# Optimization experiments

Measured on AMD Instinct MI355X. Metric: run time of the kernel, lower is better.

## Reference

```python
import jax, jax.numpy as jnp
import numpy as np

B, S, D = 2, 4096, 1024
EPS = 1e-05


def setup_inputs() -> dict:
    key = jax.random.key(0)
    ks = jax.random.split(key, 7)
    x = jax.random.normal(ks[0], (B, S, D), dtype=jnp.float32)
    gamma = jnp.ones((D,), dtype=jnp.float32)
    wq, wk, wv, wa, wg, wo = (jax.random.normal(k, (D, D), dtype=jnp.float32) for k in ks[1:7])
    return {"x": x, "gamma": gamma, "wq": wq, "wk": wk, "wv": wv, "wa": wa, "wg": wg, "wo": wo}


def _rmsnorm(x, gamma):
    # original uses sum of squares (not mean) with scale = sqrt(dim)
    ss = jnp.sum(jnp.square(x), axis=-1, keepdims=True)
    inv = jax.lax.rsqrt(ss + EPS)
    return inv * x * gamma * (x.shape[-1] ** 0.5)


def _gate_loop_operator(kv, q, a):
    def binop(e_i, e_j):
        a_i, kv_i = e_i
        a_j, kv_j = e_j
        return (a_j * a_i, a_j * kv_i + kv_j)
    _, y = jax.lax.associative_scan(binop, (a, kv), axis=1)
    return q * y


def reference(x, gamma, wq, wk, wv, wa, wg, wo):
    x = _rmsnorm(x, gamma)
    q = x @ wq
    k = x @ wk
    v = x @ wv
    a = jax.nn.sigmoid(x @ wa)
    g = x @ wg
    kv = k * v
    y = _gate_loop_operator(kv, q, a)
    y = y * jax.nn.silu(g)
    return y @ wo
```

## Files before the change

kernel.cpp:

```cpp
#include <hip/hip_runtime.h>
#include <hip/hip_bf16.h>
#include <cstdint>
#include <cstddef>


typedef __bf16 bf16x8 __attribute__((ext_vector_type(8)));
typedef float f32x4 __attribute__((ext_vector_type(4)));

__device__ __forceinline__ void gload_lds16(const void* g, void* l) {
  __builtin_amdgcn_global_load_lds(
      (const __attribute__((address_space(1))) void*)g,
      (__attribute__((address_space(3))) void*)l,
      16, 0, 0);
}

__global__ __launch_bounds__(256) void wconv_k(
    const float* __restrict__ wq, const float* __restrict__ wk,
    const float* __restrict__ wv, const float* __restrict__ wa,
    const float* __restrict__ wg, const float* __restrict__ wo,
    __hip_bfloat16* __restrict__ wcatT, __hip_bfloat16* __restrict__ woT) {
  __shared__ float t[32][33];
  const float* src;
  __hip_bfloat16* dst;
  switch (blockIdx.z) {
    case 0: src = wq; dst = wcatT; break;
    case 1: src = wk; dst = wcatT + (size_t)1024 * 1024; break;
    case 2: src = wv; dst = wcatT + (size_t)2048 * 1024; break;
    case 3: src = wg; dst = wcatT + (size_t)3072 * 1024; break;
    case 4: src = wa; dst = wcatT + (size_t)4096 * 1024; break;
    default: src = wo; dst = woT; break;
  }
  const int n0 = blockIdx.x * 32;
  const int k0 = blockIdx.y * 32;
  const int tx = threadIdx.x, ty = threadIdx.y;
#pragma unroll
  for (int i = 0; i < 32; i += 8)
    t[ty + i][tx] = src[(size_t)(k0 + ty + i) * 1024 + n0 + tx];
  __syncthreads();
#pragma unroll
  for (int i = 0; i < 32; i += 8)
    dst[(size_t)(n0 + ty + i) * 1024 + k0 + tx] = __float2bfloat16(t[tx][ty + i]);
}

__global__ __launch_bounds__(256) void rmsnorm_k(
    const float* __restrict__ x, const float* __restrict__ gamma,
    __hip_bfloat16* __restrict__ xn) {
  const int row = blockIdx.x;
  const int tid = threadIdx.x;
  const float4 xv = ((const float4*)(x + (size_t)row * 1024))[tid];
  float ss = xv.x * xv.x + xv.y * xv.y + xv.z * xv.z + xv.w * xv.w;
#pragma unroll
  for (int off = 32; off >= 1; off >>= 1) ss += __shfl_xor(ss, off, 64);
  __shared__ float wss[4];
  if ((tid & 63) == 0) wss[tid >> 6] = ss;
  __syncthreads();
  const float total = wss[0] + wss[1] + wss[2] + wss[3];
  const float scale = rsqrtf(total + 1e-5f) * 32.0f;
  const float4 gv = ((const float4*)gamma)[tid];
  union { __hip_bfloat16 h[4]; ushort4 u; } ob;
  ob.h[0] = __float2bfloat16(xv.x * gv.x * scale);
  ob.h[1] = __float2bfloat16(xv.y * gv.y * scale);
  ob.h[2] = __float2bfloat16(xv.z * gv.z * scale);
  ob.h[3] = __float2bfloat16(xv.w * gv.w * scale);
  ((ushort4*)(xn + (size_t)row * 1024))[tid] = ob.u;
}

__global__ __launch_bounds__(256) void gemm128(
    const __hip_bfloat16* __restrict__ A, const __hip_bfloat16* __restrict__ Bt,
    int M, int N, int K,
    __hip_bfloat16* __restrict__ outb, int ldb, int nbcols,
    float* __restrict__ outf, int ldf) {
  __shared__ __align__(16) unsigned short As[3 * 4096];
  __shared__ __align__(16) unsigned short Bs[3 * 4096];

  const int tid = threadIdx.x;
  const int nwg = gridDim.x * gridDim.y;
  const int bid = blockIdx.y * gridDim.x + blockIdx.x;
  const int swz = (bid & 7) * (nwg >> 3) + (bid >> 3);
  const int brow = (swz / gridDim.x) * 128;
  const int bcol = (swz % gridDim.x) * 128;

  const unsigned short* Ag = (const unsigned short*)A + (size_t)brow * K;
  const unsigned short* Bg = (const unsigned short*)Bt + (size_t)bcol * K;

  const int srow = tid >> 2;
  const int gch8 = (((tid & 3) ^ ((tid >> 3) & 3)) << 3);

  auto stageAB = [&](int sl, int slot) {
    unsigned short* dA = As + slot * 4096;
    unsigned short* dB = Bs + slot * 4096;
    const int k0 = sl << 5;
    gload_lds16(Ag + (size_t)srow * K + k0 + gch8, dA + tid * 8);
    gload_lds16(Ag + (size_t)(srow + 64) * K + k0 + gch8, dA + 2048 + tid * 8);
    gload_lds16(Bg + (size_t)srow * K + k0 + gch8, dB + tid * 8);
    gload_lds16(Bg + (size_t)(srow + 64) * K + k0 + gch8, dB + 2048 + tid * 8);
  };

  const int lane = tid & 63;
  const int wid = tid >> 6;
  const int wr = wid >> 1;
  const int wc = wid & 1;
  const int l16 = lane & 15;
  const int k8 = lane >> 4;

  int aoff[4], boff[4];
#pragma unroll
  for (int m = 0; m < 4; ++m) {
    const int r = wr * 64 + m * 16 + l16;
    aoff[m] = r * 32 + ((k8 ^ ((r >> 1) & 3)) << 3);
  }
#pragma unroll
  for (int n = 0; n < 4; ++n) {
    const int r = wc * 64 + n * 16 + l16;
    boff[n] = r * 32 + ((k8 ^ ((r >> 1) & 3)) << 3);
  }

  f32x4 acc[4][4];
#pragma unroll
  for (int m = 0; m < 4; ++m)
#pragma unroll
    for (int n = 0; n < 4; ++n) acc[m][n] = (f32x4){0.f, 0.f, 0.f, 0.f};

  const int NS = K >> 5;
  stageAB(0, 0);
  stageAB(1, 1);
  asm volatile("s_waitcnt vmcnt(4)" ::: "memory");
  __builtin_amdgcn_s_barrier();

  int rs = 0, ws = 2;
  for (int s = 0; s < NS; ++s) {
    if (s + 2 < NS) stageAB(s + 2, ws);
    const unsigned short* As_s = As + rs * 4096;
    const unsigned short* Bs_s = Bs + rs * 4096;
    bf16x8 af[4], bfr[4];
#pragma unroll
    for (int m = 0; m < 4; ++m) af[m] = *(const bf16x8*)(As_s + aoff[m]);
#pragma unroll
    for (int n = 0; n < 4; ++n) bfr[n] = *(const bf16x8*)(Bs_s + boff[n]);
    __builtin_amdgcn_s_setprio(1);
#pragma unroll
    for (int m = 0; m < 4; ++m)
#pragma unroll
      for (int n = 0; n < 4; ++n)
        acc[m][n] = __builtin_amdgcn_mfma_f32_16x16x32_bf16(af[m], bfr[n], acc[m][n], 0, 0, 0);
    __builtin_amdgcn_s_setprio(0);
    if (s <= NS - 3) {
      asm volatile("s_waitcnt vmcnt(4)" ::: "memory");
      __builtin_amdgcn_s_barrier();
    } else if (s == NS - 2) {
      asm volatile("s_waitcnt vmcnt(0)" ::: "memory");
      __builtin_amdgcn_s_barrier();
    }
    rs = (rs == 2) ? 0 : rs + 1;
    ws = (ws == 2) ? 0 : ws + 1;
  }

  const int mb = brow + wr * 64 + k8 * 4;
  const int nb = bcol + wc * 64 + l16;
#pragma unroll
  for (int m = 0; m < 4; ++m) {
#pragma unroll
    for (int n = 0; n < 4; ++n) {
      const int col = nb + n * 16;
#pragma unroll
      for (int r = 0; r < 4; ++r) {
        const int row = mb + m * 16 + r;
        const float v = acc[m][n][r];
        if (col < nbcols) {
          outb[(size_t)row * ldb + col] = __float2bfloat16(v);
        } else {
          outf[(size_t)row * ldf + (col - nbcols)] = v;
        }
      }
    }
  }
}

__global__ __launch_bounds__(256) void scan_pass1(
    const __hip_bfloat16* __restrict__ qkvg, const float* __restrict__ apre,
    float* __restrict__ Asum, float* __restrict__ Ysum) {
  const int bc = blockIdx.x;
  const int d = blockIdx.y * 256 + threadIdx.x;
  const size_t rowbase = (size_t)(bc >> 5) * 4096 + (size_t)(bc & 31) * 128;
  float y = 0.f, Ap = 1.f;
  for (int s = 0; s < 128; ++s) {
    const size_t r = rowbase + s;
    const float kk = __bfloat162float(qkvg[r * 4096 + 1024 + d]);
    const float vv = __bfloat162float(qkvg[r * 4096 + 2048 + d]);
    const float ap = apre[r * 1024 + d];
    const float a = 1.f / (1.f + __expf(-ap));
    y = fmaf(a, y, kk * vv);
    Ap *= a;
  }
  Asum[(size_t)bc * 1024 + d] = Ap;
  Ysum[(size_t)bc * 1024 + d] = y;
}

__global__ __launch_bounds__(256) void scan_pass2(
    const float* __restrict__ Asum, const float* __restrict__ Ysum,
    float* __restrict__ carry) {
  const int idx = blockIdx.x * 256 + threadIdx.x;
  const int b = idx >> 10, d = idx & 1023;
  float y = 0.f;
  for (int c = 0; c < 32; ++c) {
    const size_t o = (size_t)(b * 32 + c) * 1024 + d;
    carry[o] = y;
    y = fmaf(Asum[o], y, Ysum[o]);
  }
}

__global__ __launch_bounds__(256) void scan_pass3(
    const __hip_bfloat16* __restrict__ qkvg, const float* __restrict__ apre,
    const float* __restrict__ carry, __hip_bfloat16* __restrict__ yact) {
  const int bc = blockIdx.x;
  const int d = blockIdx.y * 256 + threadIdx.x;
  const size_t rowbase = (size_t)(bc >> 5) * 4096 + (size_t)(bc & 31) * 128;
  float y = carry[(size_t)bc * 1024 + d];
  for (int s = 0; s < 128; ++s) {
    const size_t r = rowbase + s;
    const float qq = __bfloat162float(qkvg[r * 4096 + d]);
    const float kk = __bfloat162float(qkvg[r * 4096 + 1024 + d]);
    const float vv = __bfloat162float(qkvg[r * 4096 + 2048 + d]);
    const float gg = __bfloat162float(qkvg[r * 4096 + 3072 + d]);
    const float ap = apre[r * 1024 + d];
    const float a = 1.f / (1.f + __expf(-ap));
    y = fmaf(a, y, kk * vv);
    const float sg = 1.f / (1.f + __expf(-gg));
    yact[r * 1024 + d] = __float2bfloat16(qq * y * gg * sg);
  }
}

extern "C" void kernel_launch(void* const* d_in, const int* in_sizes, int n_in,
                              void* d_out, int out_size, void* d_ws, size_t ws_size,
                              hipStream_t stream) {
  const float* x     = (const float*)d_in[0];
  const float* gamma = (const float*)d_in[1];
  const float* wq    = (const float*)d_in[2];
  const float* wk    = (const float*)d_in[3];
  const float* wv    = (const float*)d_in[4];
  const float* wa    = (const float*)d_in[5];
  const float* wg    = (const float*)d_in[6];
  const float* wo    = (const float*)d_in[7];
  float* out = (float*)d_out;

  char* ws = (char*)d_ws;
  __hip_bfloat16* wcatT = (__hip_bfloat16*)(ws);
  __hip_bfloat16* woT   = (__hip_bfloat16*)(ws + 10485760);
  __hip_bfloat16* xn    = (__hip_bfloat16*)(ws + 12582912);
  __hip_bfloat16* qkvg  = (__hip_bfloat16*)(ws + 29360128);
  float*          apre  = (float*)(ws + 96468992);
  __hip_bfloat16* yact  = (__hip_bfloat16*)(ws + 130023424);
  float*          Asum  = (float*)(ws + 146800640);
  float*          Ysum  = (float*)(ws + 147062784);
  float*          carry = (float*)(ws + 147324928);

  wconv_k<<<dim3(32, 32, 6), dim3(32, 8, 1), 0, stream>>>(wq, wk, wv, wa, wg, wo, wcatT, woT);
  rmsnorm_k<<<dim3(8192), dim3(256), 0, stream>>>(x, gamma, xn);
  gemm128<<<dim3(40, 64), dim3(256), 0, stream>>>(
      xn, wcatT, 8192, 5120, 1024, qkvg, 4096, 4096, apre, 1024);
  scan_pass1<<<dim3(64, 4), dim3(256), 0, stream>>>(qkvg, apre, Asum, Ysum);
  scan_pass2<<<dim3(8), dim3(256), 0, stream>>>(Asum, Ysum, carry);
  scan_pass3<<<dim3(64, 4), dim3(256), 0, stream>>>(qkvg, apre, carry, yact);
  gemm128<<<dim3(8, 64), dim3(256), 0, stream>>>(
      yact, woT, 8192, 1024, 1024, (__hip_bfloat16*)nullptr, 0, 0, out, 1024);
}
```

Before: 222.8 us.

## Add 256x256 ping-pong pipelined GEMM for the fused QKVGA projection

Adds a new bf16 GEMM kernel with 256x256 output tiles, 512 threads and 8 waves, each wave owning a 128x64 sub-tile. The K loop is split into quarter-tile phases, with LDS fragment loads, async global-to-LDS staging, barriers and s_setprio around the MFMA bursts so memory traffic overlaps compute. The large fused input projection (N=5120) now uses this kernel instead of the 128x128 one. The aim is more data reuse per loaded tile and better MFMA utilisation, at the cost of a 128 KB LDS footprint, heavy register use and only 640 workgroups, which may leave the GPU's CUs unevenly loaded.

```diff
diff --git a/kernel.cpp b/kernel.cpp
--- a/kernel.cpp
+++ b/kernel.cpp
@@ -13,6 +13,13 @@
       (__attribute__((address_space(3))) void*)l,
       16, 0, 0);
 }
+
+__device__ __forceinline__ bf16x8 ldfrag(const unsigned short* p) {
+  return *(const bf16x8*)p;
+}
+
+#define MFMA16(acc_, a_, b_) \
+  acc_ = __builtin_amdgcn_mfma_f32_16x16x32_bf16(a_, b_, acc_, 0, 0, 0)
 
 __global__ __launch_bounds__(256) void wconv_k(
     const float* __restrict__ wq, const float* __restrict__ wk,
@@ -63,6 +70,265 @@
   ob.h[2] = __float2bfloat16(xv.z * gv.z * scale);
   ob.h[3] = __float2bfloat16(xv.w * gv.w * scale);
   ((ushort4*)(xn + (size_t)row * 1024))[tid] = ob.u;
+}
+
+__global__ __launch_bounds__(512, 2) void gemm256p(
+    const __hip_bfloat16* __restrict__ A, const __hip_bfloat16* __restrict__ Bt,
+    int M, int N, int K,
+    __hip_bfloat16* __restrict__ outb, int ldb, int nbcols,
+    float* __restrict__ outf, int ldf) {
+  __shared__ __align__(16) unsigned short lds[65536];
+  unsigned short* Asl = lds;
+  unsigned short* Bsl = lds + 32768;
+
+  const int tid = threadIdx.x;
+  const int nwg = gridDim.x * gridDim.y;
+  const int bid = blockIdx.y * gridDim.x + blockIdx.x;
+  const int swz = (bid & 7) * (nwg >> 3) + (bid >> 3);
+  const int brow = (swz / gridDim.x) * 256;
+  const int bcol = (swz % gridDim.x) * 256;
+
+  const unsigned short* Ag = (const unsigned short*)A + (size_t)brow * K;
+  const unsigned short* Bg = (const unsigned short*)Bt + (size_t)bcol * K;
+
+  const int sr = tid >> 3;
+  const int sc = tid & 7;
+
+  auto stage = [&](unsigned short* dst, const unsigned short* G, int ht, int T) {
+#pragma unroll
+    for (int j = 0; j < 2; ++j) {
+      const int row = sr + j * 64;
+      gload_lds16(G + (size_t)(ht * 128 + row) * K + T * 64 + ((sc ^ (row & 7)) << 3),
+                  dst + row * 64 + sc * 8);
+    }
+  };
+
+  const int lane = tid & 63;
+  const int wid = tid >> 6;
+  const int wr = wid >> 2;
+  const int wc = wid & 3;
+  const int l16 = lane & 15;
+  const int k8 = lane >> 4;
+
+  int aoff[8], boff[4];
+#pragma unroll
+  for (int m = 0; m < 8; ++m) {
+    const int row = wr * 128 + m * 16 + l16;
+    const int ht = row >> 7, hr = row & 127;
+    aoff[m] = ht * 8192 + hr * 64 + ((k8 ^ (hr & 7)) << 3);
+  }
+#pragma unroll
+  for (int n = 0; n < 4; ++n) {
+    const int row = wc * 64 + n * 16 + l16;
+    const int ht = row >> 7, hr = row & 127;
+    boff[n] = ht * 8192 + hr * 64 + ((k8 ^ (hr & 7)) << 3);
+  }
+
+  f32x4 acc[8][4];
+#pragma unroll
+  for (int m = 0; m < 8; ++m)
+#pragma unroll
+    for (int n = 0; n < 4; ++n) acc[m][n] = (f32x4){0.f, 0.f, 0.f, 0.f};
+
+  const int NT = K >> 6;
+
+  stage(Asl, Ag, 0, 0);          stage(Asl + 8192, Ag, 1, 0);
+  stage(Bsl, Bg, 0, 0);          stage(Bsl + 8192, Bg, 1, 0);
+  stage(Bsl + 16384, Bg, 0, 1);  stage(Bsl + 16384 + 8192, Bg, 1, 1);
+  asm volatile("s_waitcnt vmcnt(4)" ::: "memory");
+  __builtin_amdgcn_s_barrier();
+
+  bf16x8 aL[4][2], aH[4][2], bL[2][2], bH[2][2];
+
+  for (int i = 0; i < NT / 2; ++i) {
+    const int T1 = 2 * i + 1, T2 = 2 * i + 2, T3 = 2 * i + 3;
+    const unsigned short* A0 = Asl;
+    const unsigned short* B0 = Bsl;
+    const unsigned short* A1 = Asl + 16384;
+    const unsigned short* B1 = Bsl + 16384;
+
+#pragma unroll
+    for (int m = 0; m < 4; ++m) {
+      aL[m][0] = ldfrag(A0 + aoff[m]);
+      aL[m][1] = ldfrag(A0 + (aoff[m] ^ 32));
+    }
+#pragma unroll
+    for (int n = 0; n < 2; ++n) {
+      bL[n][0] = ldfrag(B0 + boff[n]);
+      bL[n][1] = ldfrag(B0 + (boff[n] ^ 32));
+    }
+    stage(Asl + 16384, Ag, 0, T1);
+    asm volatile("s_waitcnt lgkmcnt(8)" ::: "memory");
+    __builtin_amdgcn_s_barrier();
+    asm volatile("s_waitcnt lgkmcnt(0)" ::: "memory");
+    __builtin_amdgcn_s_setprio(1);
+#pragma unroll
+    for (int m = 0; m < 4; ++m)
+#pragma unroll
+      for (int n = 0; n < 2; ++n) {
+        MFMA16(acc[m][n], aL[m][0], bL[n][0]);
+        MFMA16(acc[m][n], aL[m][1], bL[n][1]);
+      }
+    __builtin_amdgcn_s_setprio(0);
+    __builtin_amdgcn_s_barrier();
+
+#pragma unroll
+    for (int n = 0; n < 2; ++n) {
+      bH[n][0] = ldfrag(B0 + boff[2 + n]);
+      bH[n][1] = ldfrag(B0 + (boff[2 + n] ^ 32));
+    }
+    stage(Asl + 16384 + 8192, Ag, 1, T1);
+    __builtin_amdgcn_s_barrier();
+    asm volatile("s_waitcnt lgkmcnt(0)" ::: "memory");
+    __builtin_amdgcn_s_setprio(1);
+#pragma unroll
+    for (int m = 0; m < 4; ++m)
+#pragma unroll
+      for (int n = 0; n < 2; ++n) {
+        MFMA16(acc[m][2 + n], aL[m][0], bH[n][0]);
+        MFMA16(acc[m][2 + n], aL[m][1], bH[n][1]);
+      }
+    __builtin_amdgcn_s_setprio(0);
+    __builtin_amdgcn_s_barrier();
+
+#pragma unroll
+    for (int m = 0; m < 4; ++m) {
+      aH[m][0] = ldfrag(A0 + aoff[4 + m]);
+      aH[m][1] = ldfrag(A0 + (aoff[4 + m] ^ 32));
+    }
+    if (T2 < NT) stage(Bsl, Bg, 0, T2);
+    __builtin_amdgcn_s_barrier();
+    asm volatile("s_waitcnt lgkmcnt(0)" ::: "memory");
+    __builtin_amdgcn_s_setprio(1);
+#pragma unroll
+    for (int m = 0; m < 4; ++m)
+#pragma unroll
+      for (int n = 0; n < 2; ++n) {
+        MFMA16(acc[4 + m][2 + n], aH[m][0], bH[n][0]);
+        MFMA16(acc[4 + m][2 + n], aH[m][1], bH[n][1]);
+      }
+    __builtin_amdgcn_s_setprio(0);
+    __builtin_amdgcn_s_barrier();
+
+    if (T2 < NT) {
+      stage(Bsl + 8192, Bg, 1, T2);
+      asm volatile("s_waitcnt vmcnt(4)" ::: "memory");
+    } else {
+      asm volatile("s_waitcnt vmcnt(0)" ::: "memory");
+    }
+    __builtin_amdgcn_s_barrier();
+    __builtin_amdgcn_s_setprio(1);
+#pragma unroll
+    for (int m = 0; m < 4; ++m)
+#pragma unroll
+      for (int n = 0; n < 2; ++n) {
+        MFMA16(acc[4 + m][n], aH[m][0], bL[n][0]);
+        MFMA16(acc[4 + m][n], aH[m][1], bL[n][1]);
+      }
+    __builtin_amdgcn_s_setprio(0);
+    __builtin_amdgcn_s_barrier();
+
+#pragma unroll
+    for (int m = 0; m < 4; ++m) {
+      aL[m][0] = ldfrag(A1 + aoff[m]);
+      aL[m][1] = ldfrag(A1 + (aoff[m] ^ 32));
+    }
+#pragma unroll
+    for (int n = 0; n < 2; ++n) {
+      bL[n][0] = ldfrag(B1 + boff[n]);
+      bL[n][1] = ldfrag(B1 + (boff[n] ^ 32));
+    }
+    if (T2 < NT) stage(Asl, Ag, 0, T2);
+    asm volatile("s_waitcnt lgkmcnt(8)" ::: "memory");
+    __builtin_amdgcn_s_barrier();
+    asm volatile("s_waitcnt lgkmcnt(0)" ::: "memory");
+    __builtin_amdgcn_s_setprio(1);
+#pragma unroll
+    for (int m = 0; m < 4; ++m)
+#pragma unroll
+      for (int n = 0; n < 2; ++n) {
+        MFMA16(acc[m][n], aL[m][0], bL[n][0]);
+        MFMA16(acc[m][n], aL[m][1], bL[n][1]);
+      }
+    __builtin_amdgcn_s_setprio(0);
+    __builtin_amdgcn_s_barrier();
+
+#pragma unroll
+    for (int n = 0; n < 2; ++n) {
+      bH[n][0] = ldfrag(B1 + boff[2 + n]);
+      bH[n][1] = ldfrag(B1 + (boff[2 + n] ^ 32));
+    }
+    if (T2 < NT) stage(Asl + 8192, Ag, 1, T2);
+    __builtin_amdgcn_s_barrier();
+    asm volatile("s_waitcnt lgkmcnt(0)" ::: "memory");
+    __builtin_amdgcn_s_setprio(1);
+#pragma unroll
+    for (int m = 0; m < 4; ++m)
+#pragma unroll
+      for (int n = 0; n < 2; ++n) {
+        MFMA16(acc[m][2 + n], aL[m][0], bH[n][0]);
+        MFMA16(acc[m][2 + n], aL[m][1], bH[n][1]);
+      }
+    __builtin_amdgcn_s_setprio(0);
+    __builtin_amdgcn_s_barrier();
+
+#pragma unroll
+    for (int m = 0; m < 4; ++m) {
+      aH[m][0] = ldfrag(A1 + aoff[4 + m]);
+      aH[m][1] = ldfrag(A1 + (aoff[4 + m] ^ 32));
+    }
+    if (T3 < NT) stage(Bsl + 16384, Bg, 0, T3);
+    __builtin_amdgcn_s_barrier();
+    asm volatile("s_waitcnt lgkmcnt(0)" ::: "memory");
+    __builtin_amdgcn_s_setprio(1);
+#pragma unroll
+    for (int m = 0; m < 4; ++m)
+#pragma unroll
+      for (int n = 0; n < 2; ++n) {
+        MFMA16(acc[4 + m][2 + n], aH[m][0], bH[n][0]);
+        MFMA16(acc[4 + m][2 + n], aH[m][1], bH[n][1]);
+      }
+    __builtin_amdgcn_s_setprio(0);
+    __builtin_amdgcn_s_barrier();
+
+    if (T3 < NT) {
+      stage(Bsl + 16384 + 8192, Bg, 1, T3);
+      asm volatile("s_waitcnt vmcnt(4)" ::: "memory");
+    } else {
+      asm volatile("s_waitcnt vmcnt(0)" ::: "memory");
+    }
+    __builtin_amdgcn_s_barrier();
+    __builtin_amdgcn_s_setprio(1);
+#pragma unroll
+    for (int m = 0; m < 4; ++m)
+#pragma unroll
+      for (int n = 0; n < 2; ++n) {
+        MFMA16(acc[4 + m][n], aH[m][0], bL[n][0]);
+        MFMA16(acc[4 + m][n], aH[m][1], bL[n][1]);
+      }
+    __builtin_amdgcn_s_setprio(0);
+    __builtin_amdgcn_s_barrier();
+  }
+
+  const int mb = brow + wr * 128 + k8 * 4;
+  const int nb = bcol + wc * 64 + l16;
+#pragma unroll
+  for (int m = 0; m < 8; ++m) {
+#pragma unroll
+    for (int n = 0; n < 4; ++n) {
+      const int col = nb + n * 16;
+#pragma unroll
+      for (int r = 0; r < 4; ++r) {
+        const int row = mb + m * 16 + r;
+        const float v = acc[m][n][r];
+        if (col < nbcols) {
+          outb[(size_t)row * ldb + col] = __float2bfloat16(v);
+        } else {
+          outf[(size_t)row * ldf + (col - nbcols)] = v;
+        }
+      }
+    }
+  }
 }
 
 __global__ __launch_bounds__(256) void gemm128(
@@ -256,7 +522,7 @@
 
   wconv_k<<<dim3(32, 32, 6), dim3(32, 8, 1), 0, stream>>>(wq, wk, wv, wa, wg, wo, wcatT, woT);
   rmsnorm_k<<<dim3(8192), dim3(256), 0, stream>>>(x, gamma, xn);
-  gemm128<<<dim3(40, 64), dim3(256), 0, stream>>>(
+  gemm256p<<<dim3(20, 32), dim3(512), 0, stream>>>(
       xn, wcatT, 8192, 5120, 1024, qkvg, 4096, 4096, apre, 1024);
   scan_pass1<<<dim3(64, 4), dim3(256), 0, stream>>>(qkvg, apre, Asum, Ysum);
   scan_pass2<<<dim3(8), dim3(256), 0, stream>>>(Asum, Ysum, carry);
```

Measured after the change: 207.1 us. 7.1% less time.

## Interleave k/v and q/g weight columns and use single-buffered GEMM for projection

Applied to the files above, without the earlier changes.

Weight rows are permuted during conversion so the projection GEMM emits k and v, and q and g, as adjacent bf16 pairs. The scan kernels can then fetch each pair with one 32-bit load instead of separate strided 16-bit loads, which should improve memory coalescing. The first projection GEMM also moves to a new single-stage-buffered kernel with smaller LDS use, which could raise occupancy but loses the triple-buffered prefetch overlap. The output projection still uses the original GEMM.

```diff
diff --git a/kernel.cpp b/kernel.cpp
--- a/kernel.cpp
+++ b/kernel.cpp
@@ -12,6 +12,13 @@
       (const __attribute__((address_space(1))) void*)g,
       (__attribute__((address_space(3))) void*)l,
       16, 0, 0);
+}
+
+__device__ __forceinline__ float bfhi(unsigned int u) {
+  union { unsigned int i; float f; } c; c.i = u & 0xffff0000u; return c.f;
+}
+__device__ __forceinline__ float bflo(unsigned int u) {
+  union { unsigned int i; float f; } c; c.i = u << 16; return c.f;
 }
 
 __global__ __launch_bounds__(256) void wconv_k(
@@ -22,13 +29,14 @@
   __shared__ float t[32][33];
   const float* src;
   __hip_bfloat16* dst;
+  int rmul, roff;
   switch (blockIdx.z) {
-    case 0: src = wq; dst = wcatT; break;
-    case 1: src = wk; dst = wcatT + (size_t)1024 * 1024; break;
-    case 2: src = wv; dst = wcatT + (size_t)2048 * 1024; break;
-    case 3: src = wg; dst = wcatT + (size_t)3072 * 1024; break;
-    case 4: src = wa; dst = wcatT + (size_t)4096 * 1024; break;
-    default: src = wo; dst = woT; break;
+    case 0: src = wq; dst = wcatT; rmul = 2; roff = 2048; break;
+    case 1: src = wk; dst = wcatT; rmul = 2; roff = 0;    break;
+    case 2: src = wv; dst = wcatT; rmul = 2; roff = 1;    break;
+    case 3: src = wg; dst = wcatT; rmul = 2; roff = 2049; break;
+    case 4: src = wa; dst = wcatT; rmul = 1; roff = 4096; break;
+    default: src = wo; dst = woT;  rmul = 1; roff = 0;    break;
   }
   const int n0 = blockIdx.x * 32;
   const int k0 = blockIdx.y * 32;
@@ -39,7 +47,8 @@
   __syncthreads();
 #pragma unroll
   for (int i = 0; i < 32; i += 8)
-    dst[(size_t)(n0 + ty + i) * 1024 + k0 + tx] = __float2bfloat16(t[tx][ty + i]);
+    dst[(size_t)(roff + rmul * (n0 + ty + i)) * 1024 + k0 + tx] =
+        __float2bfloat16(t[tx][ty + i]);
 }
 
 __global__ __launch_bounds__(256) void rmsnorm_k(
@@ -65,6 +74,101 @@
   ((ushort4*)(xn + (size_t)row * 1024))[tid] = ob.u;
 }
 
+__global__ __launch_bounds__(256) void gemm_sb(
+    const __hip_bfloat16* __restrict__ A, const __hip_bfloat16* __restrict__ Bt,
+    int M, int N, int K,
+    __hip_bfloat16* __restrict__ outb, int ldb, int nbcols,
+    float* __restrict__ outf, int ldf) {
+  __shared__ __align__(16) unsigned short As[4096];
+  __shared__ __align__(16) unsigned short Bs[4096];
+
+  const int tid = threadIdx.x;
+  const int nwg = gridDim.x * gridDim.y;
+  const int bid = blockIdx.y * gridDim.x + blockIdx.x;
+  const int swz = (bid & 7) * (nwg >> 3) + (bid >> 3);
+  const int brow = (swz / gridDim.x) * 128;
+  const int bcol = (swz % gridDim.x) * 128;
+
+  const unsigned short* Ag = (const unsigned short*)A + (size_t)brow * K;
+  const unsigned short* Bg = (const unsigned short*)Bt + (size_t)bcol * K;
+
+  const int srow = tid >> 2;
+  const int gch8 = (((tid & 3) ^ ((tid >> 3) & 3)) << 3);
+
+  auto stage = [&](int s) {
+    const int k0 = s << 5;
+    gload_lds16(Ag + (size_t)srow * K + k0 + gch8, As + tid * 8);
+    gload_lds16(Ag + (size_t)(srow + 64) * K + k0 + gch8, As + 2048 + tid * 8);
+    gload_lds16(Bg + (size_t)srow * K + k0 + gch8, Bs + tid * 8);
+    gload_lds16(Bg + (size_t)(srow + 64) * K + k0 + gch8, Bs + 2048 + tid * 8);
+  };
+
+  const int lane = tid & 63;
+  const int wid = tid >> 6;
+  const int wr = wid >> 1;
+  const int wc = wid & 1;
+  const int l16 = lane & 15;
+  const int k8 = lane >> 4;
+
+  int aoff[4], boff[4];
+#pragma unroll
+  for (int m = 0; m < 4; ++m) {
+    const int r = wr * 64 + m * 16 + l16;
+    aoff[m] = r * 32 + ((k8 ^ ((r >> 1) & 3)) << 3);
+  }
+#pragma unroll
+  for (int n = 0; n < 4; ++n) {
+    const int r = wc * 64 + n * 16 + l16;
+    boff[n] = r * 32 + ((k8 ^ ((r >> 1) & 3)) << 3);
+  }
+
+  f32x4 acc[4][4];
+#pragma unroll
+  for (int m = 0; m < 4; ++m)
+#pragma unroll
+    for (int n = 0; n < 4; ++n) acc[m][n] = (f32x4){0.f, 0.f, 0.f, 0.f};
+
+  const int NS = K >> 5;
+  stage(0);
+  for (int s = 0; s < NS; ++s) {
+    __syncthreads();
+    bf16x8 af[4], bfr[4];
+#pragma unroll
+    for (int m = 0; m < 4; ++m) af[m] = *(const bf16x8*)(As + aoff[m]);
+#pragma unroll
+    for (int n = 0; n < 4; ++n) bfr[n] = *(const bf16x8*)(Bs + boff[n]);
+#pragma unroll
+    for (int m = 0; m < 4; ++m)
+#pragma unroll
+      for (int n = 0; n < 4; ++n)
+        acc[m][n] = __builtin_amdgcn_mfma_f32_16x16x32_bf16(af[m], bfr[n], acc[m][n], 0, 0, 0);
+    if (s + 1 < NS) {
+      __syncthreads();
+      stage(s + 1);
+    }
+  }
+
+  const int mb = brow + wr * 64 + k8 * 4;
+  const int nb = bcol + wc * 64 + l16;
+#pragma unroll
+  for (int m = 0; m < 4; ++m) {
+#pragma unroll
+    for (int n = 0; n < 4; ++n) {
+      const int col = nb + n * 16;
+#pragma unroll
+      for (int r = 0; r < 4; ++r) {
+        const int row = mb + m * 16 + r;
+        const float v = acc[m][n][r];
+        if (col < nbcols) {
+          outb[(size_t)row * ldb + col] = __float2bfloat16(v);
+        } else {
+          outf[(size_t)row * ldf + (col - nbcols)] = v;
+        }
+      }
+    }
+  }
+}
+
 __global__ __launch_bounds__(256) void gemm128(
     const __hip_bfloat16* __restrict__ A, const __hip_bfloat16* __restrict__ Bt,
     int M, int N, int K,
@@ -182,14 +286,14 @@
   const int bc = blockIdx.x;
   const int d = blockIdx.y * 256 + threadIdx.x;
   const size_t rowbase = (size_t)(bc >> 5) * 4096 + (size_t)(bc & 31) * 128;
+  const unsigned int* kvp = (const unsigned int*)qkvg;
   float y = 0.f, Ap = 1.f;
   for (int s = 0; s < 128; ++s) {
     const size_t r = rowbase + s;
-    const float kk = __bfloat162float(qkvg[r * 4096 + 1024 + d]);
-    const float vv = __bfloat162float(qkvg[r * 4096 + 2048 + d]);
+    const unsigned int kv = kvp[r * 2048 + d];
     const float ap = apre[r * 1024 + d];
     const float a = 1.f / (1.f + __expf(-ap));
-    y = fmaf(a, y, kk * vv);
+    y = fmaf(a, y, bflo(kv) * bfhi(kv));
     Ap *= a;
   }
   Asum[(size_t)bc * 1024 + d] = Ap;
@@ -216,17 +320,17 @@
   const int d = blockIdx.y * 256 + threadIdx.x;
   const size_t rowbase = (size_t)(bc >> 5) * 4096 + (size_t)(bc & 31) * 128;
   float y = carry[(size_t)bc * 1024 + d];
+  const unsigned int* kvp = (const unsigned int*)qkvg;
   for (int s = 0; s < 128; ++s) {
     const size_t r = rowbase + s;
-    const float qq = __bfloat162float(qkvg[r * 4096 + d]);
-    const float kk = __bfloat162float(qkvg[r * 4096 + 1024 + d]);
-    const float vv = __bfloat162float(qkvg[r * 4096 + 2048 + d]);
-    const float gg = __bfloat162float(qkvg[r * 4096 + 3072 + d]);
+    const unsigned int kv = kvp[r * 2048 + d];
+    const unsigned int qg = kvp[r * 2048 + 1024 + d];
     const float ap = apre[r * 1024 + d];
     const float a = 1.f / (1.f + __expf(-ap));
-    y = fmaf(a, y, kk * vv);
+    y = fmaf(a, y, bflo(kv) * bfhi(kv));
+    const float gg = bfhi(qg);
     const float sg = 1.f / (1.f + __expf(-gg));
-    yact[r * 1024 + d] = __float2bfloat16(qq * y * gg * sg);
+    yact[r * 1024 + d] = __float2bfloat16(bflo(qg) * y * gg * sg);
   }
 }
 
@@ -256,7 +360,7 @@
 
   wconv_k<<<dim3(32, 32, 6), dim3(32, 8, 1), 0, stream>>>(wq, wk, wv, wa, wg, wo, wcatT, woT);
   rmsnorm_k<<<dim3(8192), dim3(256), 0, stream>>>(x, gamma, xn);
-  gemm128<<<dim3(40, 64), dim3(256), 0, stream>>>(
+  gemm_sb<<<dim3(40, 64), dim3(256), 0, stream>>>(
       xn, wcatT, 8192, 5120, 1024, qkvg, 4096, 4096, apre, 1024);
   scan_pass1<<<dim3(64, 4), dim3(256), 0, stream>>>(qkvg, apre, Asum, Ysum);
   scan_pass2<<<dim3(8), dim3(256), 0, stream>>>(Asum, Ysum, carry);
```

Result: slower. 234.3 us (+5.2%).
